# Kernel optimization log

Measured on AMD Instinct MI355X. Metric: run time of the kernel, lower is better.

The kernel has to match this reference:

```python
import jax, jax.numpy as jnp
import numpy as np
import math

B, S, D_MODEL, H = 2, 2048, 2048, 16
HD = D_MODEL // H  # head_dim = 128


def setup_inputs() -> dict:
    key = jax.random.key(0)
    ks = jax.random.split(key, 10)
    x = jax.random.normal(ks[0], (B, S, D_MODEL), dtype=jnp.float32)
    # RoPE tables: interleaved-pair layout matching rotate_half (adjacent dims form pairs)
    inv_freq = 1.0 / (10000.0 ** (jnp.arange(0, HD, 2, dtype=jnp.float32) / HD))  # [HD/2]
    angles = jnp.arange(S, dtype=jnp.float32)[:, None] * inv_freq[None, :]        # [S, HD/2]
    angles = jnp.repeat(angles, 2, axis=-1)                                       # [S, HD]
    cos, sin = jnp.cos(angles), jnp.sin(angles)
    # causal mask (1 = keep), broadcastable to [B,H,S,S]
    attn_mask = jnp.tril(jnp.ones((S, S), dtype=bool))[None, None]
    scale = 1.0 / math.sqrt(D_MODEL)
    Wq = jax.random.normal(ks[1], (D_MODEL, D_MODEL), dtype=jnp.float32) * scale
    Wk = jax.random.normal(ks[2], (D_MODEL, D_MODEL), dtype=jnp.float32) * scale
    Wv = jax.random.normal(ks[3], (D_MODEL, D_MODEL), dtype=jnp.float32) * scale
    Wo = jax.random.normal(ks[4], (D_MODEL, D_MODEL), dtype=jnp.float32) * scale
    bq = jnp.zeros((D_MODEL,), jnp.float32)
    bk = jnp.zeros((D_MODEL,), jnp.float32)
    bv = jnp.zeros((D_MODEL,), jnp.float32)
    bo = jnp.zeros((D_MODEL,), jnp.float32)
    return {"x": x, "cos": cos, "sin": sin, "attn_mask": attn_mask,
            "Wq": Wq, "bq": bq, "Wk": Wk, "bk": bk, "Wv": Wv, "bv": bv, "Wo": Wo, "bo": bo}


def _rotate_half(x):
    # pairs adjacent dims: (x0,x1) -> (-x1,x0)
    xr = x.reshape(*x.shape[:-1], -1, 2)
    x1, x2 = xr[..., 0], xr[..., 1]
    return jnp.stack([-x2, x1], axis=-1).reshape(x.shape)


def reference(x, cos, sin, attn_mask, Wq, bq, Wk, bk, Wv, bv, Wo, bo):
    b, s, _ = x.shape
    q = (x @ Wq.T + bq).reshape(b, s, H, HD).transpose(0, 2, 1, 3)  # [B,H,S,HD]
    k = (x @ Wk.T + bk).reshape(b, s, H, HD).transpose(0, 2, 1, 3)
    v = (x @ Wv.T + bv).reshape(b, s, H, HD).transpose(0, 2, 1, 3)
    c = cos[None, None]  # [1,1,S,HD]
    sn = sin[None, None]
    q = q * c + _rotate_half(q) * sn
    k = k * c + _rotate_half(k) * sn
    scores = jnp.einsum('bhqd,bhkd->bhqk', q, k) / math.sqrt(HD)  # [B,H,S,S]
    scores = jnp.where(attn_mask, scores, -jnp.inf)
    attn = jax.nn.softmax(scores, axis=-1)
    out = jnp.einsum('bhqk,bhkd->bhqd', attn, v)  # [B,H,S,HD]
    out = out.transpose(0, 2, 1, 3).reshape(b, s, H * HD)
    return out @ Wo.T + bo
```

## Files before the change

### kernel.cpp

```cpp
#include <hip/hip_runtime.h>
#include <math.h>

typedef __attribute__((ext_vector_type(8))) __bf16 bf16x8;
typedef __attribute__((ext_vector_type(4))) float f32x4;
typedef __attribute__((ext_vector_type(4))) unsigned short us4;
typedef unsigned short u16;
typedef unsigned int u32;

#define DEVI static __device__ __forceinline__

DEVI u16 f2bf(float f) {
  union { float f; unsigned u; } v; v.f = f;
  unsigned r = v.u + 0x7fffu + ((v.u >> 16) & 1u);
  return (u16)(r >> 16);
}

DEVI void async16(const void* g, void* l) {
  __builtin_amdgcn_global_load_lds((const __attribute__((address_space(1))) void*)g,
                                   (__attribute__((address_space(3))) void*)l, 16, 0, 0);
}

DEVI u32 pkbf(float lo, float hi) {
  u32 r;
  asm("v_cvt_pk_bf16_f32 %0, %1, %2" : "=v"(r) : "v"(lo), "v"(hi));
  return r;
}

__global__ __launch_bounds__(256)
void cast_all(const float* __restrict__ x,
              const float* __restrict__ wq, const float* __restrict__ wk,
              const float* __restrict__ wv, const float* __restrict__ wo,
              u16* __restrict__ xb, u16* __restrict__ wqb, u16* __restrict__ wkb,
              u16* __restrict__ wvb, u16* __restrict__ wob)
{
  const int NX = 4096 * 2048, NW = 2048 * 2048;
  int i = (blockIdx.x * 256 + threadIdx.x) * 4;
  const float* src; u16* dst; int off;
  if (i < NX)               { src = x;  dst = xb;  off = i; }
  else if (i < NX + NW)     { src = wq; dst = wqb; off = i - NX; }
  else if (i < NX + 2 * NW) { src = wk; dst = wkb; off = i - NX - NW; }
  else if (i < NX + 3 * NW) { src = wv; dst = wvb; off = i - NX - 2 * NW; }
  else                      { src = wo; dst = wob; off = i - NX - 3 * NW; }
  float4 v = *(const float4*)(src + off);
  us4 o = { f2bf(v.x), f2bf(v.y), f2bf(v.z), f2bf(v.w) };
  *(us4*)(dst + off) = o;
}

template<int MODE>
__global__ __launch_bounds__(256, 3)
void gemm_bt(const u16* __restrict__ A, const u16* __restrict__ B,
             const float* __restrict__ bias,
             const float* __restrict__ cosT, const float* __restrict__ sinT,
             void* __restrict__ outp)
{
  __shared__ __align__(16) u16 As[8192];
  __shared__ __align__(16) u16 Bs[8192];
  const int t = threadIdx.x, w = t >> 6, lane = t & 63;
  const int lrow = lane & 15, lk8 = (lane >> 4) * 8;
  const int brow = blockIdx.y * 128, bcol = blockIdx.x * 128;
  const int wr = (w >> 1) * 64, wc = (w & 1) * 64;

  u32 sA[4], sB[4];
#pragma unroll
  for (int r = 0; r < 4; ++r) {
    const int q = (r * 256 + t) * 16;
    const int row = q >> 7;
    const int cb = (q ^ ((row & 7) << 4)) & 127;
    sA[r] = (u32)((brow + row) * 2048 + (cb >> 1));
    sB[r] = (u32)((bcol + row) * 2048 + (cb >> 1));
  }

  int offA[4][2], offB[4][2];
#pragma unroll
  for (int m = 0; m < 4; ++m)
#pragma unroll
    for (int kk = 0; kk < 2; ++kk) {
      int row = wr + m * 16 + lrow;
      offA[m][kk] = (row * 128 + (kk * 32 + lk8) * 2) ^ ((row & 7) << 4);
      row = wc + m * 16 + lrow;
      offB[m][kk] = (row * 128 + (kk * 32 + lk8) * 2) ^ ((row & 7) << 4);
    }

  f32x4 acc[4][4] = {};

  for (int k0 = 0; k0 < 2048; k0 += 64) {
#pragma unroll
    for (int r = 0; r < 4; ++r) {
      async16(A + sA[r] + k0, (char*)As + (r * 256 + t) * 16);
      async16(B + sB[r] + k0, (char*)Bs + (r * 256 + t) * 16);
    }
    __syncthreads();
#pragma unroll
    for (int kk = 0; kk < 2; ++kk) {
      bf16x8 a[4], b[4];
#pragma unroll
      for (int m = 0; m < 4; ++m) a[m] = *(const bf16x8*)((char*)As + offA[m][kk]);
#pragma unroll
      for (int n = 0; n < 4; ++n) b[n] = *(const bf16x8*)((char*)Bs + offB[n][kk]);
#pragma unroll
      for (int m = 0; m < 4; ++m)
#pragma unroll
        for (int n = 0; n < 4; ++n)
          acc[m][n] = __builtin_amdgcn_mfma_f32_16x16x32_bf16(a[m], b[n], acc[m][n], 0, 0, 0);
    }
    __syncthreads();
  }

#pragma unroll
  for (int mi = 0; mi < 4; ++mi) {
#pragma unroll
    for (int ni = 0; ni < 4; ++ni) {
      f32x4 v = acc[mi][ni];
      const int row0 = brow + wr + mi * 16 + (lane >> 4) * 4;
      const int col = bcol + wc + ni * 16 + lrow;
      if constexpr (MODE == 3) {
        float* O = (float*)outp;
        const float bv = bias[col];
#pragma unroll
        for (int r = 0; r < 4; ++r)
          O[(size_t)(row0 + r) * 2048 + col] = v[r] + bv;
      } else if constexpr (MODE == 0 || MODE == 1) {
        u16* O = (u16*)outp;
        const float bv = bias[col];
        const int h = col >> 7, d = col & 127;
        const float sgn = (d & 1) ? 1.f : -1.f;
        const float QSCL = 0.08838834764831845f * 1.44269504088896340f;
#pragma unroll
        for (int r = 0; r < 4; ++r) {
          const int row = row0 + r, bb = row >> 11, s = row & 2047;
          float q = v[r] + bv;
          float p = __shfl_xor(q, 1);
          float o = q * cosT[s * 128 + d] + sgn * p * sinT[s * 128 + d];
          if constexpr (MODE == 0) o *= QSCL;
          u16* base = O + ((size_t)(bb * 16 + h) * 2048 + s) * 128;
          if constexpr (MODE == 0) {
            base[d] = f2bf(o);
          } else {
            *(u16*)((char*)base + (((unsigned)(d << 1)) ^ (unsigned)((s & 7) << 4))) = f2bf(o);
          }
        }
      } else {
        u16* O = (u16*)outp;
        const float bv = bias[col];
        const int h = col >> 7, d = col & 127;
        const int bb = row0 >> 11, s = row0 & 2047;
        us4 ov;
#pragma unroll
        for (int r = 0; r < 4; ++r) ov[r] = f2bf(v[r] + bv);
        const int l = s & 63;
        const int kt = l >> 4, g2 = (l >> 2) & 3;
        const int c = ((kt >> 1) << 5) + (g2 << 3) + ((kt & 1) << 2);
        u16* base = O + ((size_t)(bb * 16 + h) * 128 + d) * 2048 + (s & ~63);
        *(us4*)((char*)base + ((unsigned)(c << 1) ^ (unsigned)((d & 7) << 4))) = ov;
      }
    }
  }
}

__global__ __launch_bounds__(256, 2)
void attn_fwd(const u16* __restrict__ Q, const u16* __restrict__ K,
              const u16* __restrict__ Vt, u16* __restrict__ AO)
{
  __shared__ __align__(16) u16 Ks[2][64 * 128];
  __shared__ __align__(16) u16 Vs[2][128 * 64];
  const int t = threadIdx.x, w = t >> 6, lane = t & 63;
  const int lrow = lane & 15, g = lane >> 4, lk8 = g * 8;
  const int id = blockIdx.x;
  const int half = id >> 8, r8 = id & 255;
  const int bh = (r8 & 7) | (((r8 >> 3) & 3) << 3);
  const int pr = r8 >> 5;
  const int qt = half ? (15 - pr) : pr;
  const u16* Qg = Q + (size_t)bh * 2048 * 128;
  const u16* Kg = K + (size_t)bh * 2048 * 128;
  const u16* Vg = Vt + (size_t)bh * 128 * 2048;
  const int bb = bh >> 4, h = bh & 15;

  const int qw = qt * 128 + w * 32;
  const int nkv = 2 * (qt + 1);
  const int qg0 = qw + lrow;

  bf16x8 qf[2][4];
#pragma unroll
  for (int s2 = 0; s2 < 2; ++s2)
#pragma unroll
    for (int c = 0; c < 4; ++c)
      qf[s2][c] = *(const bf16x8*)(Qg + (size_t)(qw + s2 * 16 + lrow) * 128 + lk8 + c * 32);

  f32x4 acc[2][8] = {};
  float m[2] = { -1e30f, -1e30f }, lsum[2] = { 0.f, 0.f };

  auto stage = [&](int i, int b) {
#pragma unroll
    for (int r = 0; r < 4; ++r) {
      int e = (r * 256 + t) * 8;
      async16(Kg + (size_t)i * 8192 + e, &Ks[b][r * 2048 + w * 512]);
      async16(Vg + (size_t)(e >> 6) * 2048 + i * 64 + (e & 63), &Vs[b][r * 2048 + w * 512]);
    }
  };

  stage(0, 0);
  for (int i = 0; i < nkv; ++i) {
    const int cur = i & 1;
    const bool pfch = (i + 1) < nkv;
    if (pfch) stage(i + 1, cur ^ 1);
    if (pfch) asm volatile("s_waitcnt vmcnt(8)" ::: "memory");
    else      asm volatile("s_waitcnt vmcnt(0)" ::: "memory");
    __builtin_amdgcn_s_barrier();
    __builtin_amdgcn_sched_barrier(0);

    f32x4 sc[2][4];
    __builtin_amdgcn_s_setprio(1);
#pragma unroll
    for (int kt = 0; kt < 4; ++kt) {
      f32x4 s0 = {}, s1 = {};
      const int krow = kt * 16 + lrow;
      const char* kbase = (const char*)(&Ks[cur][krow * 128]);
      const unsigned sw = (unsigned)((krow & 7) << 4);
#pragma unroll
      for (int c = 0; c < 4; ++c) {
        bf16x8 kf = *(const bf16x8*)(kbase + ((unsigned)((lk8 + c * 32) << 1) ^ sw));
        s0 = __builtin_amdgcn_mfma_f32_16x16x32_bf16(kf, qf[0][c], s0, 0, 0, 0);
        s1 = __builtin_amdgcn_mfma_f32_16x16x32_bf16(kf, qf[1][c], s1, 0, 0, 0);
      }
      sc[0][kt] = s0; sc[1][kt] = s1;
    }
    __builtin_amdgcn_s_setprio(0);

    const bool guard = (i * 64 + 63) > qw;
    bf16x8 pb[2][2];
#pragma unroll
    for (int s2 = 0; s2 < 2; ++s2) {
      const int qgs = qg0 + s2 * 16;
      float p[4][4];
      if (guard) {
#pragma unroll
        for (int kt = 0; kt < 4; ++kt)
#pragma unroll
          for (int r = 0; r < 4; ++r) {
            int kg = i * 64 + kt * 16 + g * 4 + r;
            p[kt][r] = (kg > qgs) ? -1e30f : sc[s2][kt][r];
          }
      } else {
#pragma unroll
        for (int kt = 0; kt < 4; ++kt)
#pragma unroll
          for (int r = 0; r < 4; ++r) p[kt][r] = sc[s2][kt][r];
      }

      float mm = p[0][0];
#pragma unroll
      for (int kt = 0; kt < 4; ++kt)
#pragma unroll
        for (int r = 0; r < 4; ++r) mm = fmaxf(mm, p[kt][r]);
      mm = fmaxf(mm, __shfl_xor(mm, 16));
      mm = fmaxf(mm, __shfl_xor(mm, 32));

      float rs = 0.f;
      if (__any(mm > m[s2] + 8.f)) {
        const float mn = fmaxf(m[s2], mm);
        const float corr = exp2f(m[s2] - mn);
        m[s2] = mn;
#pragma unroll
        for (int kt = 0; kt < 4; ++kt)
#pragma unroll
          for (int r = 0; r < 4; ++r) { p[kt][r] = exp2f(p[kt][r] - m[s2]); rs += p[kt][r]; }
        rs += __shfl_xor(rs, 16);
        rs += __shfl_xor(rs, 32);
        lsum[s2] = lsum[s2] * corr + rs;
#pragma unroll
        for (int nt = 0; nt < 8; ++nt)
#pragma unroll
          for (int r = 0; r < 4; ++r) acc[s2][nt][r] *= corr;
      } else {
#pragma unroll
        for (int kt = 0; kt < 4; ++kt)
#pragma unroll
          for (int r = 0; r < 4; ++r) { p[kt][r] = exp2f(p[kt][r] - m[s2]); rs += p[kt][r]; }
        rs += __shfl_xor(rs, 16);
        rs += __shfl_xor(rs, 32);
        lsum[s2] += rs;
      }

#pragma unroll
      for (int kc = 0; kc < 2; ++kc) {
        union { u32 d[4]; bf16x8 v; } u;
        u.d[0] = pkbf(p[2 * kc][0], p[2 * kc][1]);
        u.d[1] = pkbf(p[2 * kc][2], p[2 * kc][3]);
        u.d[2] = pkbf(p[2 * kc + 1][0], p[2 * kc + 1][1]);
        u.d[3] = pkbf(p[2 * kc + 1][2], p[2 * kc + 1][3]);
        pb[s2][kc] = u.v;
      }
    }

    __builtin_amdgcn_s_setprio(1);
#pragma unroll
    for (int nt = 0; nt < 8; ++nt) {
      const int vrow = nt * 16 + lrow;
      const char* vbase = (const char*)(&Vs[cur][vrow * 64]);
      const unsigned sw2 = (unsigned)((vrow & 7) << 4);
#pragma unroll
      for (int kc = 0; kc < 2; ++kc) {
        bf16x8 vf = *(const bf16x8*)(vbase + ((unsigned)((lk8 + kc * 32) << 1) ^ sw2));
        acc[0][nt] = __builtin_amdgcn_mfma_f32_16x16x32_bf16(vf, pb[0][kc], acc[0][nt], 0, 0, 0);
        acc[1][nt] = __builtin_amdgcn_mfma_f32_16x16x32_bf16(vf, pb[1][kc], acc[1][nt], 0, 0, 0);
      }
    }
    __builtin_amdgcn_s_setprio(0);
    __builtin_amdgcn_s_barrier();
  }

#pragma unroll
  for (int s2 = 0; s2 < 2; ++s2) {
    const float inv_l = 1.f / lsum[s2];
    const int qgs = qg0 + s2 * 16;
#pragma unroll
    for (int nt = 0; nt < 8; ++nt) {
      us4 ov;
#pragma unroll
      for (int r = 0; r < 4; ++r) ov[r] = f2bf(acc[s2][nt][r] * inv_l);
      *(us4*)(AO + ((size_t)(bb * 2048 + qgs)) * 2048 + h * 128 + nt * 16 + g * 4) = ov;
    }
  }
}

extern "C" void kernel_launch(void* const* d_in, const int* in_sizes, int n_in,
                              void* d_out, int out_size, void* d_ws, size_t ws_size,
                              hipStream_t stream) {
  const float* x    = (const float*)d_in[0];
  const float* cosT = (const float*)d_in[1];
  const float* sinT = (const float*)d_in[2];
  const float* Wq   = (const float*)d_in[4];
  const float* bq   = (const float*)d_in[5];
  const float* Wk   = (const float*)d_in[6];
  const float* bk   = (const float*)d_in[7];
  const float* Wv   = (const float*)d_in[8];
  const float* bv   = (const float*)d_in[9];
  const float* Wo   = (const float*)d_in[10];
  const float* bo   = (const float*)d_in[11];
  float* out = (float*)d_out;

  char* ws = (char*)d_ws;
  u16* xb  = (u16*)(ws);
  u16* Wqb = (u16*)(ws + (16u << 20));
  u16* Wkb = (u16*)(ws + (24u << 20));
  u16* Wvb = (u16*)(ws + (32u << 20));
  u16* Wob = (u16*)(ws + (40u << 20));
  u16* Qb  = (u16*)(ws + (48u << 20));
  u16* Kb  = (u16*)(ws + (64u << 20));
  u16* Vtb = (u16*)(ws + (80u << 20));
  u16* AOb = (u16*)(ws + (96u << 20));

  cast_all<<<24576, 256, 0, stream>>>(x, Wq, Wk, Wv, Wo, xb, Wqb, Wkb, Wvb, Wob);

  dim3 gg(16, 32);
  gemm_bt<0><<<gg, 256, 0, stream>>>(xb, Wqb, bq, cosT, sinT, (void*)Qb);
  gemm_bt<1><<<gg, 256, 0, stream>>>(xb, Wkb, bk, cosT, sinT, (void*)Kb);
  gemm_bt<2><<<gg, 256, 0, stream>>>(xb, Wvb, bv, nullptr, nullptr, (void*)Vtb);

  attn_fwd<<<512, 256, 0, stream>>>(Qb, Kb, Vtb, AOb);

  gemm_bt<3><<<gg, 256, 0, stream>>>(AOb, Wob, bo, nullptr, nullptr, (void*)out);
}
```

Baseline: 262.5 us.

## Pair short and long causal query tiles per block to balance attention work

Each attention block now processes two 64-row query tiles, p and 31-p, instead of one 128-row tile. Every wave holds 16 rows from each tile. The blocks iterate over 32-p KV tiles, and the MFMAs and softmax for the short tile are predicated off once it passes its diagonal. This gives every block nearly equal work under the causal mask, removing tail imbalance across blocks. The cost is that waves sit partly idle on the masked half for many iterations, which adds branch overhead and some divergence inside the loop.

After: 263.6 us. No clear change (+0.4%).

```diff
diff --git a/kernel.cpp b/kernel.cpp
--- a/kernel.cpp
+++ b/kernel.cpp
@@ -168,23 +168,24 @@
   const int id = blockIdx.x;
   const int half = id >> 8, r8 = id & 255;
   const int bh = (r8 & 7) | (((r8 >> 3) & 3) << 3);
-  const int pr = r8 >> 5;
-  const int qt = half ? (15 - pr) : pr;
+  const int j = r8 >> 5;
+  const int p = half ? (15 - j) : j;
+  const int qt0 = p, qt1 = 31 - p;
+  const int nkv = 32 - p;
   const u16* Qg = Q + (size_t)bh * 2048 * 128;
   const u16* Kg = K + (size_t)bh * 2048 * 128;
   const u16* Vg = Vt + (size_t)bh * 128 * 2048;
   const int bb = bh >> 4, h = bh & 15;
 
-  const int qw = qt * 128 + w * 32;
-  const int nkv = 2 * (qt + 1);
-  const int qg0 = qw + lrow;
+  const int qw0 = qt0 * 64 + w * 16, qw1 = qt1 * 64 + w * 16;
+  const int qg0 = qw0 + lrow, qg1 = qw1 + lrow;
 
   bf16x8 qf[2][4];
 #pragma unroll
-  for (int s2 = 0; s2 < 2; ++s2)
-#pragma unroll
-    for (int c = 0; c < 4; ++c)
-      qf[s2][c] = *(const bf16x8*)(Qg + (size_t)(qw + s2 * 16 + lrow) * 128 + lk8 + c * 32);
+  for (int c = 0; c < 4; ++c) {
+    qf[0][c] = *(const bf16x8*)(Qg + (size_t)(qw0 + lrow) * 128 + lk8 + c * 32);
+    qf[1][c] = *(const bf16x8*)(Qg + (size_t)(qw1 + lrow) * 128 + lk8 + c * 32);
+  }
 
   f32x4 acc[2][8] = {};
   float m[2] = { -1e30f, -1e30f }, lsum[2] = { 0.f, 0.f };
@@ -208,6 +209,8 @@
     __builtin_amdgcn_s_barrier();
     __builtin_amdgcn_sched_barrier(0);
 
+    const bool act0 = (i <= p);
+
     f32x4 sc[2][4];
     __builtin_amdgcn_s_setprio(1);
 #pragma unroll
@@ -219,39 +222,41 @@
 #pragma unroll
       for (int c = 0; c < 4; ++c) {
         bf16x8 kf = *(const bf16x8*)(kbase + ((unsigned)((lk8 + c * 32) << 1) ^ sw));
-        s0 = __builtin_amdgcn_mfma_f32_16x16x32_bf16(kf, qf[0][c], s0, 0, 0, 0);
         s1 = __builtin_amdgcn_mfma_f32_16x16x32_bf16(kf, qf[1][c], s1, 0, 0, 0);
+        if (act0) s0 = __builtin_amdgcn_mfma_f32_16x16x32_bf16(kf, qf[0][c], s0, 0, 0, 0);
       }
       sc[0][kt] = s0; sc[1][kt] = s1;
     }
     __builtin_amdgcn_s_setprio(0);
 
-    const bool guard = (i * 64 + 63) > qw;
     bf16x8 pb[2][2];
 #pragma unroll
     for (int s2 = 0; s2 < 2; ++s2) {
-      const int qgs = qg0 + s2 * 16;
-      float p[4][4];
+      if (s2 == 0 && !act0) continue;
+      const int qws = s2 ? qw1 : qw0;
+      const int qgs = s2 ? qg1 : qg0;
+      const bool guard = (i * 64 + 63) > qws;
+      float pv[4][4];
       if (guard) {
 #pragma unroll
         for (int kt = 0; kt < 4; ++kt)
 #pragma unroll
           for (int r = 0; r < 4; ++r) {
             int kg = i * 64 + kt * 16 + g * 4 + r;
-            p[kt][r] = (kg > qgs) ? -1e30f : sc[s2][kt][r];
+            pv[kt][r] = (kg > qgs) ? -1e30f : sc[s2][kt][r];
           }
       } else {
 #pragma unroll
         for (int kt = 0; kt < 4; ++kt)
 #pragma unroll
-          for (int r = 0; r < 4; ++r) p[kt][r] = sc[s2][kt][r];
-      }
-
-      float mm = p[0][0];
+          for (int r = 0; r < 4; ++r) pv[kt][r] = sc[s2][kt][r];
+      }
+
+      float mm = pv[0][0];
 #pragma unroll
       for (int kt = 0; kt < 4; ++kt)
 #pragma unroll
-        for (int r = 0; r < 4; ++r) mm = fmaxf(mm, p[kt][r]);
+        for (int r = 0; r < 4; ++r) mm = fmaxf(mm, pv[kt][r]);
       mm = fmaxf(mm, __shfl_xor(mm, 16));
       mm = fmaxf(mm, __shfl_xor(mm, 32));
 
@@ -263,7 +268,7 @@
 #pragma unroll
         for (int kt = 0; kt < 4; ++kt)
 #pragma unroll
-          for (int r = 0; r < 4; ++r) { p[kt][r] = exp2f(p[kt][r] - m[s2]); rs += p[kt][r]; }
+          for (int r = 0; r < 4; ++r) { pv[kt][r] = exp2f(pv[kt][r] - m[s2]); rs += pv[kt][r]; }
         rs += __shfl_xor(rs, 16);
         rs += __shfl_xor(rs, 32);
         lsum[s2] = lsum[s2] * corr + rs;
@@ -275,7 +280,7 @@
 #pragma unroll
         for (int kt = 0; kt < 4; ++kt)
 #pragma unroll
-          for (int r = 0; r < 4; ++r) { p[kt][r] = exp2f(p[kt][r] - m[s2]); rs += p[kt][r]; }
+          for (int r = 0; r < 4; ++r) { pv[kt][r] = exp2f(pv[kt][r] - m[s2]); rs += pv[kt][r]; }
         rs += __shfl_xor(rs, 16);
         rs += __shfl_xor(rs, 32);
         lsum[s2] += rs;
@@ -284,10 +289,10 @@
 #pragma unroll
       for (int kc = 0; kc < 2; ++kc) {
         union { u32 d[4]; bf16x8 v; } u;
-        u.d[0] = pkbf(p[2 * kc][0], p[2 * kc][1]);
-        u.d[1] = pkbf(p[2 * kc][2], p[2 * kc][3]);
-        u.d[2] = pkbf(p[2 * kc + 1][0], p[2 * kc + 1][1]);
-        u.d[3] = pkbf(p[2 * kc + 1][2], p[2 * kc + 1][3]);
+        u.d[0] = pkbf(pv[2 * kc][0], pv[2 * kc][1]);
+        u.d[1] = pkbf(pv[2 * kc][2], pv[2 * kc][3]);
+        u.d[2] = pkbf(pv[2 * kc + 1][0], pv[2 * kc + 1][1]);
+        u.d[3] = pkbf(pv[2 * kc + 1][2], pv[2 * kc + 1][3]);
         pb[s2][kc] = u.v;
       }
     }
@@ -301,8 +306,9 @@
 #pragma unroll
       for (int kc = 0; kc < 2; ++kc) {
         bf16x8 vf = *(const bf16x8*)(vbase + ((unsigned)((lk8 + kc * 32) << 1) ^ sw2));
-        acc[0][nt] = __builtin_amdgcn_mfma_f32_16x16x32_bf16(vf, pb[0][kc], acc[0][nt], 0, 0, 0);
         acc[1][nt] = __builtin_amdgcn_mfma_f32_16x16x32_bf16(vf, pb[1][kc], acc[1][nt], 0, 0, 0);
+        if (act0)
+          acc[0][nt] = __builtin_amdgcn_mfma_f32_16x16x32_bf16(vf, pb[0][kc], acc[0][nt], 0, 0, 0);
       }
     }
     __builtin_amdgcn_s_setprio(0);
@@ -312,7 +318,7 @@
 #pragma unroll
   for (int s2 = 0; s2 < 2; ++s2) {
     const float inv_l = 1.f / lsum[s2];
-    const int qgs = qg0 + s2 * 16;
+    const int qgs = s2 ? qg1 : qg0;
 #pragma unroll
     for (int nt = 0; nt < 8; ++nt) {
       us4 ov;
```
